# Kernel tuning notes

Hardware: AMD Instinct MI355X
Metric: run time of the kernel (lower is better)

## Reference

```python
import jax, jax.numpy as jnp
import numpy as np

EPS = 1e-5

def setup_inputs() -> dict:
    key = jax.random.key(0)
    k1, k2, k3 = jax.random.split(key, 3)
    B, T, F = 64, 512, 1024
    x = jax.random.normal(k1, (B, T, F), dtype=jnp.float32)
    # Linear(width_time, width_time): torch stores weight as (out, in)
    W = jax.random.normal(k2, (T, T), dtype=jnp.float32) * (1.0 / np.sqrt(T))
    b = jax.random.normal(k3, (T,), dtype=jnp.float32) * 0.01
    gamma = jnp.ones((1,), dtype=jnp.float32)
    beta = jnp.zeros((1,), dtype=jnp.float32)
    return {"x": x, "W": W, "b": b, "gamma": gamma, "beta": beta}


def reference(x, W, b, gamma, beta):
    # TSBatchNorm2d: BatchNorm2d(num_features=1) over x.unsqueeze(1)
    # -> stats over all (B, T, F) elements, scalar affine (training-mode batch stats).
    mean = jnp.mean(x)
    var = jnp.var(x)
    y = (x - mean) * jax.lax.rsqrt(var + EPS) * gamma[0] + beta[0]
    # transpose (B,T,F) -> (B,F,T), Linear over time dim, ReLU
    # (dropout is identity in eval mode), transpose back, residual add.
    yt = jnp.swapaxes(y, 1, 2)                      # (B, F, T)
    h = jnp.einsum('bft,ut->bfu', yt, W) + b        # Linear: y @ W.T + b
    h = jax.nn.relu(h)
    return x + jnp.swapaxes(h, 1, 2)                # (B, T, F)
```

## Files before the change

### kernel.cpp

```cpp
#include <hip/hip_runtime.h>
#include <stdint.h>

#define TDIM 512
#define FDIM 1024
#define NTOT 33554432.0f
#define EPS  1e-5f

typedef unsigned short ushort_t;
typedef unsigned short ushort4_t __attribute__((ext_vector_type(4)));
typedef short short8 __attribute__((ext_vector_type(8)));
typedef float floatx4 __attribute__((ext_vector_type(4)));

__device__ __forceinline__ ushort_t f2bf(float f) {
    union { float f; uint32_t u; } v; v.f = f;
    uint32_t r = (v.u + 0x7fffu + ((v.u >> 16) & 1u)) >> 16;
    return (ushort_t)r;
}

__device__ __forceinline__ void async16(const ushort_t* g, ushort_t* l) {
    __builtin_amdgcn_global_load_lds(
        (const __attribute__((address_space(1))) void*)g,
        (__attribute__((address_space(3))) void*)l, 16, 0, 0);
}


__global__ __launch_bounds__(256) void k_stats_transpose(
    const float* __restrict__ x, ushort_t* __restrict__ xTC,
    float2* __restrict__ partials)
{
    __shared__ ushort_t tile[64 * 128];
    __shared__ float red[8];

    int tid = threadIdx.x, bid = blockIdx.x;
    int b  = bid >> 6;
    int t0 = ((bid >> 3) & 7) << 6;
    int ft = bid & 7;
    int f0 = ft << 7;

    int r8 = tid >> 5, c8 = tid & 31;
    const float* xb = x + ((size_t)(b * TDIM + t0) * FDIM) + f0;

    float4 v[8];
#pragma unroll
    for (int p = 0; p < 8; ++p)
        v[p] = *(const float4*)(xb + (size_t)(p * 8 + r8) * FDIM + c8 * 4);

    float s = 0.f, q = 0.f;
#pragma unroll
    for (int p = 0; p < 8; ++p) {
        float4 t = v[p];
        s += t.x + t.y + t.z + t.w;
        q += t.x * t.x + t.y * t.y + t.z * t.z + t.w * t.w;
        ushort4_t pk;
        pk[0] = f2bf(t.x); pk[1] = f2bf(t.y); pk[2] = f2bf(t.z); pk[3] = f2bf(t.w);
        *(ushort4_t*)&tile[(p * 8 + r8) * 128 + c8 * 4] = pk;
    }

#pragma unroll
    for (int off = 32; off > 0; off >>= 1) {
        s += __shfl_down(s, off, 64);
        q += __shfl_down(q, off, 64);
    }
    int lane = tid & 63, w = tid >> 6;
    if (lane == 0) { red[w] = s; red[4 + w] = q; }
    __syncthreads();
    if (tid == 0) {
        partials[bid] = make_float2(red[0] + red[1] + red[2] + red[3],
                                    red[4] + red[5] + red[6] + red[7]);
    }

    int fl = tid & 127, hf = tid >> 7;
    size_t base = ((size_t)((b * 8 + ft) * 16) + (t0 >> 5) + hf) * 4096;
#pragma unroll
    for (int qq = 0; qq < 4; ++qq) {
        int tr = hf * 32 + qq * 8;
        uint32_t w0 = (uint32_t)tile[(tr + 0) * 128 + fl] | ((uint32_t)tile[(tr + 1) * 128 + fl] << 16);
        uint32_t w1 = (uint32_t)tile[(tr + 2) * 128 + fl] | ((uint32_t)tile[(tr + 3) * 128 + fl] << 16);
        uint32_t w2 = (uint32_t)tile[(tr + 4) * 128 + fl] | ((uint32_t)tile[(tr + 5) * 128 + fl] << 16);
        uint32_t w3 = (uint32_t)tile[(tr + 6) * 128 + fl] | ((uint32_t)tile[(tr + 7) * 128 + fl] << 16);
        uint4 o = make_uint4(w0, w1, w2, w3);
        *(uint4*)&xTC[base + (size_t)(qq * 128 + fl) * 8] = o;
    }
}

__global__ __launch_bounds__(256) void k_wcast(
    const float* __restrict__ W, ushort_t* __restrict__ WbC,
    float* __restrict__ rowsumW)
{
    __shared__ float red[4];
    int u = blockIdx.x, tid = threadIdx.x;
    float2 lv = *(const float2*)(W + (size_t)u * 512 + 2 * tid);

    int mt = u >> 7, m = u & 127;
    int kt = tid >> 4;
    int qq = (tid & 15) >> 2;
    int e  = 2 * (tid & 3);
    size_t off = ((size_t)(mt * 16 + kt)) * 4096 + (size_t)(qq * 128 + m) * 8 + e;
    uint32_t pk = (uint32_t)f2bf(lv.x) | ((uint32_t)f2bf(lv.y) << 16);
    *(uint32_t*)&WbC[off] = pk;

    float s = lv.x + lv.y;
#pragma unroll
    for (int off2 = 32; off2 > 0; off2 >>= 1) s += __shfl_down(s, off2, 64);
    int lane = tid & 63, w = tid >> 6;
    if (lane == 0) red[w] = s;
    __syncthreads();
    if (tid == 0) rowsumW[u] = red[0] + red[1] + red[2] + red[3];
}

__global__ __launch_bounds__(256) void k_reduce(
    const float2* __restrict__ partials, const float* __restrict__ rowsumW,
    const float* __restrict__ bias, const float* __restrict__ gamma,
    const float* __restrict__ beta, float* __restrict__ stats,
    float* __restrict__ d)
{
    __shared__ float red[8];
    __shared__ float sac[2];
    int tid = threadIdx.x;
    float s = 0.f, q = 0.f;
#pragma unroll
    for (int i = 0; i < 16; ++i) {
        float2 p = partials[i * 256 + tid];
        s += p.x; q += p.y;
    }
#pragma unroll
    for (int off = 32; off > 0; off >>= 1) {
        s += __shfl_down(s, off, 64);
        q += __shfl_down(q, off, 64);
    }
    int lane = tid & 63, w = tid >> 6;
    if (lane == 0) { red[w] = s; red[4 + w] = q; }
    __syncthreads();
    if (tid == 0) {
        float S = red[0] + red[1] + red[2] + red[3];
        float Q = red[4] + red[5] + red[6] + red[7];
        float mean = S * (1.f / NTOT);
        float var  = Q * (1.f / NTOT) - mean * mean;
        float a    = gamma[0] * rsqrtf(var + EPS);
        float c    = beta[0] - mean * a;
        stats[0] = a;
        sac[0] = a; sac[1] = c;
    }
    __syncthreads();
    float c = sac[1];
    d[tid]       = c * rowsumW[tid]       + bias[tid];
    d[tid + 256] = c * rowsumW[tid + 256] + bias[tid + 256];
}

__global__ __launch_bounds__(256) void k_gemm(
    const ushort_t* __restrict__ WbC, const ushort_t* __restrict__ xTC,
    const float* __restrict__ x, const float* __restrict__ d,
    const float* __restrict__ stats, float* __restrict__ out)
{
    __shared__ ulong smem_raw[2176];
    ushort_t* lds  = (ushort_t*)smem_raw;
    float*    ldsC = (float*)smem_raw;

    int tid = threadIdx.x;
    int w = tid >> 6, lane = tid & 63;

    int hb   = blockIdx.x;
    int xcd  = hb & 7;
    int rr   = hb >> 3;
    int mt   = rr & 3;
    int nt   = ((rr >> 2) << 3) + xcd;
    int b = nt >> 3, ft = nt & 7;

    int wr = w >> 1, wc = w & 1;
    int l15 = lane & 15, q = lane >> 4;

    const ushort_t* Abase = WbC + (size_t)mt * 16 * 4096;
    const ushort_t* Bbase = xTC + (size_t)(b * 8 + ft) * 16 * 4096 + tid * 8;

    int aoff = (q * 128 + wr * 64 + l15) * 8;

    floatx4 acc[4][4] = {};

    async16(Bbase,        &lds[tid * 8]);
    async16(Bbase + 2048, &lds[2048 + tid * 8]);
    __syncthreads();

    for (int kt = 0; kt < 16; ++kt) {
        int cur = (kt & 1) << 12;
        int nxt = 4096 - cur;
        if (kt < 15) {
            const ushort_t* Bg = Bbase + (kt + 1) * 4096;
            async16(Bg,        &lds[nxt + tid * 8]);
            async16(Bg + 2048, &lds[nxt + 2048 + tid * 8]);
        }

        const ushort_t* Ag = Abase + kt * 4096 + aoff;
        short8 af[4], bfr[4];
#pragma unroll
        for (int i = 0; i < 4; ++i)
            af[i] = *(const short8*)&Ag[i * 128];
#pragma unroll
        for (int j = 0; j < 4; ++j) {
            int n = wc * 64 + j * 16 + l15;
            bfr[j] = *(const short8*)&lds[cur + (q * 128 + n) * 8];
        }
#pragma unroll
        for (int i = 0; i < 4; ++i)
#pragma unroll
            for (int j = 0; j < 4; ++j)
                acc[i][j] = __builtin_amdgcn_mfma_f32_16x16x32_bf16(
                    af[i], bfr[j], acc[i][j], 0, 0, 0);

        __syncthreads();
    }

    float a = stats[0];
    int row = tid >> 3, cs = (tid & 7) * 16;
#pragma unroll
    for (int p = 0; p < 4; ++p) {
        if (wr == (p >> 1)) {
#pragma unroll
            for (int ii = 0; ii < 2; ++ii) {
                int i = (p & 1) * 2 + ii;
                int rl0 = i * 16 + q * 4 - (p & 1) * 32;
#pragma unroll
                for (int j = 0; j < 4; ++j) {
                    int col = wc * 64 + j * 16 + l15;
#pragma unroll
                    for (int r = 0; r < 4; ++r)
                        ldsC[(rl0 + r) * 132 + col] = acc[i][j][r];
                }
            }
        }
        __syncthreads();
        int tg = mt * 128 + p * 32 + row;
        float dt = d[tg];
        size_t gbase = ((size_t)b * TDIM + tg) * FDIM + ft * 128 + cs;
        const float* xr = x + gbase;
        float* orow = out + gbase;
#pragma unroll
        for (int k4 = 0; k4 < 4; ++k4) {
            float4 xv = *(const float4*)(xr + k4 * 4);
            float4 cv = *(const float4*)&ldsC[row * 132 + cs + k4 * 4];
            float4 o;
            o.x = xv.x + fmaxf(a * cv.x + dt, 0.f);
            o.y = xv.y + fmaxf(a * cv.y + dt, 0.f);
            o.z = xv.z + fmaxf(a * cv.z + dt, 0.f);
            o.w = xv.w + fmaxf(a * cv.w + dt, 0.f);
            *(float4*)(orow + k4 * 4) = o;
        }
        __syncthreads();
    }
}

extern "C" void kernel_launch(void* const* d_in, const int* in_sizes, int n_in,
                              void* d_out, int out_size, void* d_ws, size_t ws_size,
                              hipStream_t stream) {
    const float* x     = (const float*)d_in[0];
    const float* W     = (const float*)d_in[1];
    const float* bias  = (const float*)d_in[2];
    const float* gamma = (const float*)d_in[3];
    const float* beta  = (const float*)d_in[4];
    float* out = (float*)d_out;

    char* ws = (char*)d_ws;
    float*    stats    = (float*)ws;
    float*    dvec     = (float*)(ws + 1024);
    float*    rowsumW  = (float*)(ws + 4096);
    float2*   partials = (float2*)(ws + 8192);
    ushort_t* WbC      = (ushort_t*)(ws + (64 << 10));
    ushort_t* xTC      = (ushort_t*)(ws + (1 << 20));

    k_stats_transpose<<<4096, 256, 0, stream>>>(x, xTC, partials);
    k_wcast<<<512, 256, 0, stream>>>(W, WbC, rowsumW);
    k_reduce<<<1, 256, 0, stream>>>(partials, rowsumW, bias, gamma, beta, stats, dvec);
    k_gemm<<<2048, 256, 0, stream>>>(WbC, xTC, x, dvec, stats, out);
}
```

Measured before the change: 344.5 us.

## Stage A tiles through LDS with a three-deep async pipeline

The weight (A) operand is now copied into LDS with async global-to-LDS loads alongside the x tile, replacing direct global reads inside the K loop. The double buffer becomes a triple buffer, prefetching two k-steps ahead and waiting with explicit vmcnt counts and raw barriers instead of a full __syncthreads per iteration. The aim is to hide global latency for both operands behind the MFMAs. In exchange LDS use roughly triples, which can lower occupancy, and the hand-written waitcnt/barrier ordering is fragile.

```diff
diff --git a/kernel.cpp b/kernel.cpp
--- a/kernel.cpp
+++ b/kernel.cpp
@@ -152,7 +152,7 @@
     const float* __restrict__ x, const float* __restrict__ d,
     const float* __restrict__ stats, float* __restrict__ out)
 {
-    __shared__ ulong smem_raw[2176];
+    __shared__ ulong smem_raw[6144];
     ushort_t* lds  = (ushort_t*)smem_raw;
     float*    ldsC = (float*)smem_raw;
 
@@ -169,45 +169,61 @@
     int wr = w >> 1, wc = w & 1;
     int l15 = lane & 15, q = lane >> 4;
 
-    const ushort_t* Abase = WbC + (size_t)mt * 16 * 4096;
-    const ushort_t* Bbase = xTC + (size_t)(b * 8 + ft) * 16 * 4096 + tid * 8;
-
-    int aoff = (q * 128 + wr * 64 + l15) * 8;
+    const ushort_t* Ab = WbC + (size_t)mt * 16 * 4096 + tid * 8;
+    const ushort_t* Bb = xTC + (size_t)(b * 8 + ft) * 16 * 4096 + tid * 8;
 
     floatx4 acc[4][4] = {};
 
-    async16(Bbase,        &lds[tid * 8]);
-    async16(Bbase + 2048, &lds[2048 + tid * 8]);
-    __syncthreads();
-
+    auto stage = [&](int kt, int s) {
+        const ushort_t* Ag = Ab + kt * 4096;
+        const ushort_t* Bg = Bb + kt * 4096;
+        ushort_t* ls = lds + s * 8192;
+        async16(Ag,        &ls[tid * 8]);
+        async16(Ag + 2048, &ls[2048 + tid * 8]);
+        async16(Bg,        &ls[4096 + tid * 8]);
+        async16(Bg + 2048, &ls[4096 + 2048 + tid * 8]);
+    };
+
+    stage(0, 0);
+    stage(1, 1);
+
+#pragma unroll
     for (int kt = 0; kt < 16; ++kt) {
-        int cur = (kt & 1) << 12;
-        int nxt = 4096 - cur;
-        if (kt < 15) {
-            const ushort_t* Bg = Bbase + (kt + 1) * 4096;
-            async16(Bg,        &lds[nxt + tid * 8]);
-            async16(Bg + 2048, &lds[nxt + 2048 + tid * 8]);
-        }
-
-        const ushort_t* Ag = Abase + kt * 4096 + aoff;
+        if (kt < 14) {
+            stage(kt + 2, (kt + 2) % 3);
+            asm volatile("s_waitcnt vmcnt(8)" ::: "memory");
+        } else if (kt == 14) {
+            asm volatile("s_waitcnt vmcnt(4)" ::: "memory");
+        } else {
+            asm volatile("s_waitcnt vmcnt(0)" ::: "memory");
+        }
+        __builtin_amdgcn_s_barrier();
+
+        const ushort_t* cA = lds + (kt % 3) * 8192;
+        const ushort_t* cB = cA + 4096;
         short8 af[4], bfr[4];
 #pragma unroll
-        for (int i = 0; i < 4; ++i)
-            af[i] = *(const short8*)&Ag[i * 128];
+        for (int i = 0; i < 4; ++i) {
+            int m = wr * 64 + i * 16 + l15;
+            af[i] = *(const short8*)&cA[(q * 128 + m) * 8];
+        }
 #pragma unroll
         for (int j = 0; j < 4; ++j) {
             int n = wc * 64 + j * 16 + l15;
-            bfr[j] = *(const short8*)&lds[cur + (q * 128 + n) * 8];
-        }
+            bfr[j] = *(const short8*)&cB[(q * 128 + n) * 8];
+        }
+        asm volatile("s_waitcnt lgkmcnt(0)" ::: "memory");
+        __builtin_amdgcn_s_barrier();
+
 #pragma unroll
         for (int i = 0; i < 4; ++i)
 #pragma unroll
             for (int j = 0; j < 4; ++j)
                 acc[i][j] = __builtin_amdgcn_mfma_f32_16x16x32_bf16(
                     af[i], bfr[j], acc[i][j], 0, 0, 0);
-
-        __syncthreads();
-    }
+    }
+
+    __syncthreads();
 
     float a = stats[0];
     int row = tid >> 3, cs = (tid & 7) * 16;
```

After: 315.5 us. 8.4% less time.
